# Optimization experiments

Hardware: AMD Instinct MI355X
Metric: run time of the kernel (lower is better)

## Reference

```python
import jax, jax.numpy as jnp
import numpy as np

B, S, H, D, HID = 2, 2048, 16, 64, 512
INTER = 2 * HID
EPS = 1e-8
SCALE = D ** -0.5
ROPE_THETA = 10000.0


def setup_inputs() -> dict:
    key = jax.random.key(0)
    ks = jax.random.split(key, 12)
    x = jax.random.normal(ks[0], (B, S, HID), dtype=jnp.float32)
    # RoPE tables: angles[s, i] = s / theta^(2i/D), half-dim = D//2
    inv_freq = 1.0 / (ROPE_THETA ** (jnp.arange(0, D, 2, dtype=jnp.float32) / D))  # [D/2]
    ang = jnp.arange(S, dtype=jnp.float32)[:, None] * inv_freq[None, :]            # [S, D/2]
    cos_val = jnp.cos(ang)[None, None]  # [1,1,S,D/2]
    sin_val = jnp.sin(ang)[None, None]
    # additive causal mask
    i = jnp.arange(S)
    causal_mask = jnp.where(i[None, :] > i[:, None], -1e9, 0.0).astype(jnp.float32)[None, None]
    std = 0.02
    wq = jax.random.normal(ks[1], (HID, H * D), dtype=jnp.float32) * std
    wk = jax.random.normal(ks[2], (HID, H * D), dtype=jnp.float32) * std
    wv = jax.random.normal(ks[3], (HID, H * D), dtype=jnp.float32) * std
    wo = jax.random.normal(ks[4], (H * D, HID), dtype=jnp.float32) * std
    w_gate = jax.random.normal(ks[5], (HID, INTER), dtype=jnp.float32) * std
    w_up = jax.random.normal(ks[6], (HID, INTER), dtype=jnp.float32) * std
    w_down = jax.random.normal(ks[7], (INTER, HID), dtype=jnp.float32) * std
    norm1_w = jnp.ones((HID,), dtype=jnp.float32)
    norm2_w = jnp.ones((HID,), dtype=jnp.float32)
    ls_attn = jnp.full((HID,), 0.01, dtype=jnp.float32)
    ls_mlp = jnp.full((HID,), 0.01, dtype=jnp.float32)
    return {"x": x, "cos_val": cos_val, "sin_val": sin_val, "causal_mask": causal_mask,
            "wq": wq, "wk": wk, "wv": wv, "wo": wo,
            "w_gate": w_gate, "w_up": w_up, "w_down": w_down,
            "norm1_w": norm1_w, "norm2_w": norm2_w, "ls_attn": ls_attn, "ls_mlp": ls_mlp}


def _rmsnorm(x, w):
    return x * jax.lax.rsqrt(jnp.mean(x * x, axis=-1, keepdims=True) + EPS) * w


def _rope(t, cos_val, sin_val):
    # t: [B,H,S,D]; rotate-half style with concat halves
    t1, t2 = t[..., : D // 2], t[..., D // 2 :]
    return jnp.concatenate([t1 * cos_val - t2 * sin_val, t2 * cos_val + t1 * sin_val], axis=-1)


def reference(x, cos_val, sin_val, causal_mask, wq, wk, wv, wo,
              w_gate, w_up, w_down, norm1_w, norm2_w, ls_attn, ls_mlp):
    residual = x
    h = _rmsnorm(x, norm1_w)  # [B,S,HID]
    q = (h @ wq).reshape(B, S, H, D).transpose(0, 2, 1, 3)  # [B,H,S,D]
    k = (h @ wk).reshape(B, S, H, D).transpose(0, 2, 1, 3)
    v = (h @ wv).reshape(B, S, H, D).transpose(0, 2, 1, 3)
    q = _rope(q, cos_val, sin_val)
    k = _rope(k, cos_val, sin_val)
    scores = jnp.einsum("bhqd,bhkd->bhqk", q, k) * SCALE + causal_mask
    attn = jax.nn.softmax(scores, axis=-1)
    out = jnp.einsum("bhqk,bhkd->bhqd", attn, v)  # [B,H,S,D]
    out = out.transpose(0, 2, 1, 3).reshape(B, S, H * D)
    attn_out = (out @ wo) * ls_attn  # LayerScale == per-channel scale
    h = residual + attn_out
    residual2 = h
    g = _rmsnorm(h, norm2_w)
    m = jax.nn.silu(g @ w_gate) * (g @ w_up)  # SwiGLU
    m = (m @ w_down) * ls_mlp
    return residual2 + m
```

## Files before the change

kernel.cpp:

```cpp
#include <hip/hip_runtime.h>
#include <hip/hip_bf16.h>

typedef __bf16 bf16x8 __attribute__((ext_vector_type(8)));
typedef __bf16 bf16x4 __attribute__((ext_vector_type(4)));
typedef float f32x4 __attribute__((ext_vector_type(4)));

#define SEQ   2048
#define NB    2
#define NTOK  4096
#define HIDD  512
#define NHEAD 16
#define DHEAD 64
#define QKVN  3072
#define GUN   2048

#define OFF_WQKVT  0u
#define OFF_WOT    3145728u
#define OFF_WGUT   4194304u
#define OFF_WDT    6291456u
#define OFF_HB     7340032u
#define OFF_QKV    11534336u
#define OFF_ATTN   36700160u
#define OFF_H2     45088768u
#define OFF_G      53477376u
#define OFF_M      (OFF_QKV + 16777216u)

#define QSCALE 0.1803368801111731f

#if __has_builtin(__builtin_amdgcn_exp2f)
#define EXP2(x) __builtin_amdgcn_exp2f(x)
#else
#define EXP2(x) exp2f(x)
#endif

typedef unsigned int __attribute__((address_space(1))) as1_uint;
typedef unsigned int __attribute__((address_space(3))) as3_uint;
__device__ __forceinline__ void gload16(const void* g, void* l) {
    __builtin_amdgcn_global_load_lds((const as1_uint*)g, (as3_uint*)l, 16, 0, 0);
}

__global__ __launch_bounds__(256) void prep_k(
    const float* __restrict__ wq, const float* __restrict__ wk,
    const float* __restrict__ wv, const float* __restrict__ wo,
    const float* __restrict__ wg, const float* __restrict__ wu,
    const float* __restrict__ wd,
    __bf16* __restrict__ qkvT, __bf16* __restrict__ woT,
    __bf16* __restrict__ wguT, __bf16* __restrict__ wdT,
    const float* __restrict__ x, const float* __restrict__ norm1,
    __bf16* __restrict__ hb) {
    __shared__ float t[32][33];
    int bid = blockIdx.x;
    if (bid < 3584) {
        int which = bid >> 9, bx = bid & 511;
        const float* in; __bf16* out; int K, N, mode = 0, phase = 0;
        switch (which) {
            case 0: in = wq; out = qkvT;              K = 512;  N = 1024; break;
            case 1: in = wk; out = qkvT + 1024 * 512; K = 512;  N = 1024; break;
            case 2: in = wv; out = qkvT + 2048 * 512; K = 512;  N = 1024; break;
            case 3: in = wo; out = woT;               K = 1024; N = 512;  break;
            case 4: in = wg; out = wguT;              K = 512;  N = 1024; mode = 1; phase = 0; break;
            case 5: in = wu; out = wguT;              K = 512;  N = 1024; mode = 1; phase = 1; break;
            default: in = wd; out = wdT;              K = 1024; N = 512;  break;
        }
        int ntn = N >> 5;
        int n0 = (bx & (ntn - 1)) * 32;
        int k0 = (bx / ntn) * 32;
        int tx = threadIdx.x & 31, ty = threadIdx.x >> 5;
#pragma unroll
        for (int j = 0; j < 4; ++j)
            t[ty * 4 + j][tx] = in[(size_t)(k0 + ty * 4 + j) * N + n0 + tx];
        __syncthreads();
#pragma unroll
        for (int j = 0; j < 4; ++j) {
            int n = n0 + ty * 4 + j;
            int row = mode ? (((n >> 4) << 5) + phase * 16 + (n & 15)) : n;
            out[(size_t)row * K + k0 + tx] = (__bf16)t[tx][ty * 4 + j];
        }
    } else {
        int row = bid - 3584;
        int tt = threadIdx.x;
        const float* xr = x + (size_t)row * HIDD;
        float2 v = *(const float2*)&xr[tt * 2];
        float ss = v.x * v.x + v.y * v.y;
#pragma unroll
        for (int off = 32; off >= 1; off >>= 1) ss += __shfl_xor(ss, off);
        if ((tt & 63) == 0) t[0][tt >> 6] = ss;
        __syncthreads();
        float tot = t[0][0] + t[0][1] + t[0][2] + t[0][3];
        float r = rsqrtf(tot * (1.0f / HIDD) + 1e-8f);
        hb[(size_t)row * HIDD + tt * 2]     = (__bf16)(v.x * r * norm1[tt * 2]);
        hb[(size_t)row * HIDD + tt * 2 + 1] = (__bf16)(v.y * r * norm1[tt * 2 + 1]);
    }
}

__global__ __launch_bounds__(256) void rmsnorm_k(const float* __restrict__ x,
                                                 const float* __restrict__ w,
                                                 __bf16* __restrict__ out) {
    int row = blockIdx.x;
    int t = threadIdx.x;
    const float* xr = x + (size_t)row * HIDD;
    float2 v = *(const float2*)&xr[t * 2];
    float ss = v.x * v.x + v.y * v.y;
#pragma unroll
    for (int off = 32; off >= 1; off >>= 1) ss += __shfl_xor(ss, off);
    __shared__ float red[4];
    if ((t & 63) == 0) red[t >> 6] = ss;
    __syncthreads();
    float tot = red[0] + red[1] + red[2] + red[3];
    float r = rsqrtf(tot * (1.0f / HIDD) + 1e-8f);
    out[(size_t)row * HIDD + t * 2]     = (__bf16)(v.x * r * w[t * 2]);
    out[(size_t)row * HIDD + t * 2 + 1] = (__bf16)(v.y * r * w[t * 2 + 1]);
}

template <int EPI, int TM, int TN, int BK>
__global__ __launch_bounds__(256) void gemm_bt(const __bf16* __restrict__ A,
                                               const __bf16* __restrict__ Bt,
                                               int M, int N, int K,
                                               __bf16* __restrict__ Cb,
                                               float* __restrict__ Cf,
                                               const float* __restrict__ resid,
                                               const float* __restrict__ scale,
                                               const float* __restrict__ cosv,
                                               const float* __restrict__ sinv) {
    __shared__ alignas(16) __bf16 As[TM][BK];
    __shared__ alignas(16) __bf16 Bs[TN][BK];
    constexpr int MI = TM / 32, NI = TN / 32;
    constexpr int CPB = BK / 8;
    int m0 = blockIdx.y * TM, n0 = blockIdx.x * TN;
    int tid = threadIdx.x;
    int lane = tid & 63, w = tid >> 6;
    int wm = (w >> 1) * (TM / 2), wn = (w & 1) * (TN / 2);
    int lr = lane & 15, lkg = lane >> 4;
    f32x4 acc[MI][NI] = {};
    int nkt = K / BK;
    for (int kt = 0; kt < nkt; ++kt) {
        __syncthreads();
#pragma unroll
        for (int i = 0; i < (TM * BK) / 2048; ++i) {
            int c = i * 256 + tid;
            int row = c / CPB, ch = c % CPB;
            gload16(&A[(size_t)(m0 + row) * K + kt * BK + ((ch ^ (row & 7)) << 3)],
                    (__bf16*)As + c * 8);
        }
#pragma unroll
        for (int i = 0; i < (TN * BK) / 2048; ++i) {
            int c = i * 256 + tid;
            int row = c / CPB, ch = c % CPB;
            gload16(&Bt[(size_t)(n0 + row) * K + kt * BK + ((ch ^ (row & 7)) << 3)],
                    (__bf16*)Bs + c * 8);
        }
        __syncthreads();
#pragma unroll
        for (int kk = 0; kk < BK / 32; ++kk) {
            bf16x8 af[MI], bfv[NI];
#pragma unroll
            for (int mi = 0; mi < MI; ++mi) {
                int row = wm + mi * 16 + lr;
                af[mi] = *(const bf16x8*)&As[row][(((kk * 4 + lkg) ^ (row & 7)) << 3)];
            }
#pragma unroll
            for (int ni = 0; ni < NI; ++ni) {
                int row = wn + ni * 16 + lr;
                bfv[ni] = *(const bf16x8*)&Bs[row][(((kk * 4 + lkg) ^ (row & 7)) << 3)];
            }
#pragma unroll
            for (int mi = 0; mi < MI; ++mi)
#pragma unroll
                for (int ni = 0; ni < NI; ++ni)
                    acc[mi][ni] = __builtin_amdgcn_mfma_f32_16x16x32_bf16(
                        af[mi], bfv[ni], acc[mi][ni], 0, 0, 0);
        }
    }
    if (EPI == 1) {
        bool do_rope = (n0 + wn) < 2048;
        float qf = (n0 + wn) < 1024 ? QSCALE : 1.0f;
#pragma unroll
        for (int mi = 0; mi < MI; ++mi)
#pragma unroll
            for (int r = 0; r < 4; ++r) {
                int row = m0 + wm + mi * 16 + (lane >> 4) * 4 + r;
                int s = row & (SEQ - 1);
#pragma unroll
                for (int ni = 0; ni < 2; ++ni) {
                    float v1 = acc[mi][ni][r], v2 = acc[mi][ni + 2][r];
                    size_t i1 = (size_t)row * N + n0 + wn + ni * 16 + lr;
                    size_t i2 = i1 + 32;
                    if (do_rope) {
                        int d = ni * 16 + lr;
                        float c = cosv[s * 32 + d], sn = sinv[s * 32 + d];
                        Cb[i1] = (__bf16)((v1 * c - v2 * sn) * qf);
                        Cb[i2] = (__bf16)((v2 * c + v1 * sn) * qf);
                    } else {
                        Cb[i1] = (__bf16)v1;
                        Cb[i2] = (__bf16)v2;
                    }
                }
            }
    } else if (EPI == 3) {
#pragma unroll
        for (int mi = 0; mi < MI; ++mi)
#pragma unroll
            for (int r = 0; r < 4; ++r) {
                int row = m0 + wm + mi * 16 + (lane >> 4) * 4 + r;
#pragma unroll
                for (int ni = 0; ni < 4; ni += 2) {
                    float g = acc[mi][ni][r], u = acc[mi][ni + 1][r];
                    float mv = (g / (1.0f + __expf(-g))) * u;
                    int j = (((n0 + wn + ni * 16) >> 5) << 4) + lr;
                    Cb[(size_t)row * 1024 + j] = (__bf16)mv;
                }
            }
    } else {
#pragma unroll
        for (int mi = 0; mi < MI; ++mi)
#pragma unroll
            for (int ni = 0; ni < NI; ++ni)
#pragma unroll
                for (int r = 0; r < 4; ++r) {
                    int row = m0 + wm + mi * 16 + (lane >> 4) * 4 + r;
                    int col = n0 + wn + ni * 16 + lr;
                    size_t idx = (size_t)row * N + col;
                    float vv = acc[mi][ni][r];
                    if (EPI == 0) Cb[idx] = (__bf16)vv;
                    else          Cf[idx] = resid[idx] + vv * scale[col];
                }
    }
}

__global__ __launch_bounds__(256, 2) void attn_k(const __bf16* __restrict__ qkv,
                                                 __bf16* __restrict__ outp) {
    __shared__ alignas(16) __bf16 KtF[2][128 * 64];
    __shared__ alignas(16) __bf16 VtF[2][64 * 128];
    int bh = blockIdx.x;
    int b = bh >> 4, h = bh & 15;
    int qbA = blockIdx.y;
    int qbB = 31 - qbA;
    int tid = threadIdx.x, lane = tid & 63, w = tid >> 6;
    int lq = lane & 15, g = lane >> 4;
    int qr0A = qbA * 64 + w * 16, qr0B = qbB * 64 + w * 16;
    size_t tokb = (size_t)b * SEQ;
    int lastA = qbA >> 1;
    int nkbB = (qbB >> 1) + 1;

    int vslotA = ((lane >> 5) << 2) + ((lane >> 2) & 3);
    int vkeA   = (((lane >> 4) & 1) << 2) + (lane & 3);
    int vslotB = vslotA + 8;

    bf16x8 ones8;
#pragma unroll
    for (int e = 0; e < 8; ++e) ones8[e] = (__bf16)1.0f;

    bf16x8 aqA[2], aqB[2];
#pragma unroll
    for (int ks = 0; ks < 2; ++ks) {
        aqA[ks] = *(const bf16x8*)&qkv[(tokb + qr0A + lq) * QKVN + h * 64 + ks * 32 + g * 8];
        aqB[ks] = *(const bf16x8*)&qkv[(tokb + qr0B + lq) * QKVN + h * 64 + ks * 32 + g * 8];
    }

    f32x4 oaA[4] = {}, oaB[4] = {};
    f32x4 olA = {}, olB = {};
    uint4 va0, va1, vb0, vb1;
    int cur = 0;

#define STAGE(kbn, buf)                                                                            \
    {                                                                                              \
        _Pragma("unroll")                                                                          \
        for (int i = 0; i < 4; ++i) {                                                              \
            int c = i * 256 + tid;                                                                 \
            int kr = c >> 3, sw = c & 7;                                                           \
            gload16(&qkv[(tokb + (kbn) * 128 + kr) * QKVN + 1024 + h * 64 + ((sw ^ (kr & 7)) << 3)], \
                    &KtF[buf][c * 8]);                                                             \
        }                                                                                          \
        const __bf16* v0p = &qkv[(tokb + (kbn) * 128 + lane) * QKVN + 2048 + h * 64];              \
        const __bf16* v1p = v0p + (size_t)64 * QKVN;                                               \
        va0 = *(const uint4*)(v0p + (w * 2) * 8);                                                  \
        va1 = *(const uint4*)(v0p + (w * 2 + 1) * 8);                                              \
        vb0 = *(const uint4*)(v1p + (w * 2) * 8);                                                  \
        vb1 = *(const uint4*)(v1p + (w * 2 + 1) * 8);                                              \
    }

#define WRITE_V(buf)                                                                  \
    {                                                                                 \
        const __bf16* ea0 = (const __bf16*)&va0;                                      \
        const __bf16* ea1 = (const __bf16*)&va1;                                      \
        const __bf16* eb0 = (const __bf16*)&vb0;                                      \
        const __bf16* eb1 = (const __bf16*)&vb1;                                      \
        _Pragma("unroll")                                                             \
        for (int j = 0; j < 8; ++j) {                                                 \
            int dv0 = (w * 2) * 8 + j, dv1 = (w * 2 + 1) * 8 + j;                     \
            VtF[buf][dv0 * 128 + ((vslotA ^ j) << 3) + vkeA] = ea0[j];                \
            VtF[buf][dv1 * 128 + ((vslotA ^ j) << 3) + vkeA] = ea1[j];                \
            VtF[buf][dv0 * 128 + ((vslotB ^ j) << 3) + vkeA] = eb0[j];                \
            VtF[buf][dv1 * 128 + ((vslotB ^ j) << 3) + vkeA] = eb1[j];                \
        }                                                                             \
    }

#define QK_ONE(sc, aq)                                                                             \
    _Pragma("unroll")                                                                              \
    for (int jt = 0; jt < 8; ++jt)                                                                 \
        _Pragma("unroll")                                                                          \
        for (int ks = 0; ks < 2; ++ks) {                                                           \
            bf16x8 bk = *(const bf16x8*)&KtF[cur][(jt * 16 + lq) * 64 + (((ks * 4 + g) ^ (lq & 7)) << 3)]; \
            sc[jt] = __builtin_amdgcn_mfma_f32_16x16x32_bf16(bk, aq[ks], sc[jt], 0, 0, 0);         \
        }

#define MASK_ONE(sc, qr0_t, kb_t)                                                                  \
    {                                                                                              \
        int qabs = (qr0_t) + lq;                                                                   \
        _Pragma("unroll")                                                                          \
        for (int jt = 0; jt < 8; ++jt)                                                             \
            _Pragma("unroll")                                                                      \
            for (int r = 0; r < 4; ++r) {                                                          \
                int key = (kb_t) * 128 + jt * 16 + g * 4 + r;                                      \
                if (key > qabs) sc[jt][r] = -1e9f;                                                 \
            }                                                                                      \
    }

#define EXP_ONE(sc)                                                                                \
    _Pragma("unroll")                                                                              \
    for (int jt = 0; jt < 8; ++jt)                                                                 \
        _Pragma("unroll")                                                                          \
        for (int r = 0; r < 4; ++r) sc[jt][r] = EXP2(sc[jt][r]);

#define PV_ONE(sc, oa, ol)                                                                         \
    _Pragma("unroll")                                                                              \
    for (int ks2 = 0; ks2 < 4; ++ks2) {                                                            \
        bf16x8 pfv;                                                                                \
        _Pragma("unroll")                                                                          \
        for (int e = 0; e < 4; ++e) {                                                              \
            pfv[e]     = (__bf16)sc[2 * ks2][e];                                                   \
            pfv[e + 4] = (__bf16)sc[2 * ks2 + 1][e];                                               \
        }                                                                                          \
        ol = __builtin_amdgcn_mfma_f32_16x16x32_bf16(ones8, pfv, ol, 0, 0, 0);                     \
        _Pragma("unroll")                                                                          \
        for (int dt = 0; dt < 4; ++dt) {                                                           \
            bf16x8 av = *(const bf16x8*)&VtF[cur][(dt * 16 + lq) * 128 + (((ks2 * 4 + g) ^ (lq & 7)) << 3)]; \
            oa[dt] = __builtin_amdgcn_mfma_f32_16x16x32_bf16(av, pfv, oa[dt], 0, 0, 0);            \
        }                                                                                          \
    }

    STAGE(0, 0);
    WRITE_V(0);
    __syncthreads();

    for (int kb = 0; kb <= lastA; ++kb) {
        STAGE(kb + 1, cur ^ 1);
        {
            f32x4 scA[8] = {}, scB[8] = {};
            __builtin_amdgcn_s_setprio(1);
#pragma unroll
            for (int jt = 0; jt < 8; ++jt)
#pragma unroll
                for (int ks = 0; ks < 2; ++ks) {
                    bf16x8 bk = *(const bf16x8*)&KtF[cur][(jt * 16 + lq) * 64 + (((ks * 4 + g) ^ (lq & 7)) << 3)];
                    scB[jt] = __builtin_amdgcn_mfma_f32_16x16x32_bf16(bk, aqB[ks], scB[jt], 0, 0, 0);
                    scA[jt] = __builtin_amdgcn_mfma_f32_16x16x32_bf16(bk, aqA[ks], scA[jt], 0, 0, 0);
                }
            __builtin_amdgcn_s_setprio(0);
            if (kb == lastA) MASK_ONE(scA, qr0A, kb);
            EXP_ONE(scB);
            EXP_ONE(scA);
            __builtin_amdgcn_s_setprio(1);
#pragma unroll
            for (int ks2 = 0; ks2 < 4; ++ks2) {
                bf16x8 pfvA, pfvB;
#pragma unroll
                for (int e = 0; e < 4; ++e) {
                    pfvB[e]     = (__bf16)scB[2 * ks2][e];
                    pfvB[e + 4] = (__bf16)scB[2 * ks2 + 1][e];
                    pfvA[e]     = (__bf16)scA[2 * ks2][e];
                    pfvA[e + 4] = (__bf16)scA[2 * ks2 + 1][e];
                }
                olB = __builtin_amdgcn_mfma_f32_16x16x32_bf16(ones8, pfvB, olB, 0, 0, 0);
                olA = __builtin_amdgcn_mfma_f32_16x16x32_bf16(ones8, pfvA, olA, 0, 0, 0);
#pragma unroll
                for (int dt = 0; dt < 4; ++dt) {
                    bf16x8 av = *(const bf16x8*)&VtF[cur][(dt * 16 + lq) * 128 + (((ks2 * 4 + g) ^ (lq & 7)) << 3)];
                    oaB[dt] = __builtin_amdgcn_mfma_f32_16x16x32_bf16(av, pfvB, oaB[dt], 0, 0, 0);
                    oaA[dt] = __builtin_amdgcn_mfma_f32_16x16x32_bf16(av, pfvA, oaA[dt], 0, 0, 0);
                }
            }
            __builtin_amdgcn_s_setprio(0);
        }
        WRITE_V(cur ^ 1);
        __syncthreads();
        cur ^= 1;
    }
    for (int kb = lastA + 1; kb < nkbB; ++kb) {
        bool pf = (kb + 1) < nkbB;
        if (pf) STAGE(kb + 1, cur ^ 1);
        {
            f32x4 sc[8] = {};
            __builtin_amdgcn_s_setprio(1);
            QK_ONE(sc, aqB);
            __builtin_amdgcn_s_setprio(0);
            if (kb == (qbB >> 1)) MASK_ONE(sc, qr0B, kb);
            EXP_ONE(sc);
            __builtin_amdgcn_s_setprio(1);
            PV_ONE(sc, oaB, olB);
            __builtin_amdgcn_s_setprio(0);
        }
        if (pf) WRITE_V(cur ^ 1);
        __syncthreads();
        cur ^= 1;
    }

    float invA = 1.0f / olA[0], invB = 1.0f / olB[0];
#pragma unroll
    for (int dt = 0; dt < 4; ++dt) {
        bf16x4 ovA, ovB;
#pragma unroll
        for (int r = 0; r < 4; ++r) {
            ovA[r] = (__bf16)(oaA[dt][r] * invA);
            ovB[r] = (__bf16)(oaB[dt][r] * invB);
        }
        *(bf16x4*)&outp[(tokb + qr0A + lq) * 1024 + h * 64 + dt * 16 + g * 4] = ovA;
        *(bf16x4*)&outp[(tokb + qr0B + lq) * 1024 + h * 64 + dt * 16 + g * 4] = ovB;
    }
#undef STAGE
#undef WRITE_V
#undef QK_ONE
#undef MASK_ONE
#undef EXP_ONE
#undef PV_ONE
}

extern "C" void kernel_launch(void* const* d_in, const int* in_sizes, int n_in,
                              void* d_out, int out_size, void* d_ws, size_t ws_size,
                              hipStream_t stream) {
    const float* x       = (const float*)d_in[0];
    const float* cosv    = (const float*)d_in[1];
    const float* sinv    = (const float*)d_in[2];
    const float* wq      = (const float*)d_in[4];
    const float* wk      = (const float*)d_in[5];
    const float* wv      = (const float*)d_in[6];
    const float* wo      = (const float*)d_in[7];
    const float* wgate   = (const float*)d_in[8];
    const float* wup     = (const float*)d_in[9];
    const float* wdown   = (const float*)d_in[10];
    const float* norm1   = (const float*)d_in[11];
    const float* norm2   = (const float*)d_in[12];
    const float* ls_attn = (const float*)d_in[13];
    const float* ls_mlp  = (const float*)d_in[14];

    char* ws = (char*)d_ws;
    __bf16* wqkvT = (__bf16*)(ws + OFF_WQKVT);
    __bf16* woT   = (__bf16*)(ws + OFF_WOT);
    __bf16* wguT  = (__bf16*)(ws + OFF_WGUT);
    __bf16* wdT   = (__bf16*)(ws + OFF_WDT);
    __bf16* hb    = (__bf16*)(ws + OFF_HB);
    __bf16* qkvb  = (__bf16*)(ws + OFF_QKV);
    __bf16* attnb = (__bf16*)(ws + OFF_ATTN);
    float*  h2    = (float*)(ws + OFF_H2);
    __bf16* gb    = (__bf16*)(ws + OFF_G);
    __bf16* mb    = (__bf16*)(ws + OFF_M);
    float*  outf  = (float*)d_out;

    prep_k<<<7680, 256, 0, stream>>>(
        wq, wk, wv, wo, wgate, wup, wdown, wqkvT, woT, wguT, wdT, x, norm1, hb);
    gemm_bt<1, 128, 128, 64><<<dim3(QKVN / 128, NTOK / 128), 256, 0, stream>>>(
        hb, wqkvT, NTOK, QKVN, 512, qkvb, nullptr, nullptr, nullptr, cosv, sinv);
    attn_k<<<dim3(NB * NHEAD, 16), 256, 0, stream>>>(qkvb, attnb);
    gemm_bt<2, 64, 64, 128><<<dim3(HIDD / 64, NTOK / 64), 256, 0, stream>>>(
        attnb, woT, NTOK, HIDD, 1024, nullptr, h2, x, ls_attn, nullptr, nullptr);
    rmsnorm_k<<<NTOK, 256, 0, stream>>>(h2, norm2, gb);
    gemm_bt<3, 128, 128, 64><<<dim3(GUN / 128, NTOK / 128), 256, 0, stream>>>(
        gb, wguT, NTOK, GUN, 512, mb, nullptr, nullptr, nullptr, nullptr, nullptr);
    gemm_bt<2, 64, 64, 128><<<dim3(HIDD / 64, NTOK / 64), 256, 0, stream>>>(
        mb, wdT, NTOK, HIDD, 1024, nullptr, outf, h2, ls_mlp, nullptr, nullptr);
}
```

Before: 122.6 us.

## Load K fragments directly into registers instead of staging through LDS

The attention kernel drops the shared-memory K tile. Each wave now loads its K MFMA operands straight from global memory into registers (kf[8][2]), prefetched one block ahead, while V still goes through double-buffered LDS. The two query-tile loops are merged into a single loop that processes tile B and then, conditionally, tile A, using a raw s_barrier with an lgkmcnt wait. This removes the LDS write and read traffic for K and halves LDS use, but every wave redundantly loads the full K block from global or L2 and register pressure rises, which may lower occupancy.

```diff
diff --git a/kernel.cpp b/kernel.cpp
--- a/kernel.cpp
+++ b/kernel.cpp
@@ -229,7 +229,6 @@
 
 __global__ __launch_bounds__(256, 2) void attn_k(const __bf16* __restrict__ qkv,
                                                  __bf16* __restrict__ outp) {
-    __shared__ alignas(16) __bf16 KtF[2][128 * 64];
     __shared__ alignas(16) __bf16 VtF[2][64 * 128];
     int bh = blockIdx.x;
     int b = bh >> 4, h = bh & 15;
@@ -257,20 +256,22 @@
         aqB[ks] = *(const bf16x8*)&qkv[(tokb + qr0B + lq) * QKVN + h * 64 + ks * 32 + g * 8];
     }
 
+    bf16x8 kf[8][2];
     f32x4 oaA[4] = {}, oaB[4] = {};
     f32x4 olA = {}, olB = {};
     uint4 va0, va1, vb0, vb1;
     int cur = 0;
 
-#define STAGE(kbn, buf)                                                                            \
+#define LOAD_K(kbn)                                                                                \
+    _Pragma("unroll")                                                                              \
+    for (int jt = 0; jt < 8; ++jt)                                                                 \
+        _Pragma("unroll")                                                                          \
+        for (int ks = 0; ks < 2; ++ks)                                                             \
+            kf[jt][ks] = *(const bf16x8*)&qkv[(tokb + (kbn) * 128 + jt * 16 + lq) * QKVN + 1024    \
+                                              + h * 64 + ks * 32 + g * 8];
+
+#define LOAD_V(kbn)                                                                                \
     {                                                                                              \
-        _Pragma("unroll")                                                                          \
-        for (int i = 0; i < 4; ++i) {                                                              \
-            int c = i * 256 + tid;                                                                 \
-            int kr = c >> 3, sw = c & 7;                                                           \
-            gload16(&qkv[(tokb + (kbn) * 128 + kr) * QKVN + 1024 + h * 64 + ((sw ^ (kr & 7)) << 3)], \
-                    &KtF[buf][c * 8]);                                                             \
-        }                                                                                          \
         const __bf16* v0p = &qkv[(tokb + (kbn) * 128 + lane) * QKVN + 2048 + h * 64];              \
         const __bf16* v1p = v0p + (size_t)64 * QKVN;                                               \
         va0 = *(const uint4*)(v0p + (w * 2) * 8);                                                  \
@@ -295,14 +296,16 @@
         }                                                                             \
     }
 
-#define QK_ONE(sc, aq)                                                                             \
-    _Pragma("unroll")                                                                              \
-    for (int jt = 0; jt < 8; ++jt)                                                                 \
+#define QK_R(sc, aq)                                                                               \
+    {                                                                                              \
+        __builtin_amdgcn_s_setprio(1);                                                             \
         _Pragma("unroll")                                                                          \
-        for (int ks = 0; ks < 2; ++ks) {                                                           \
-            bf16x8 bk = *(const bf16x8*)&KtF[cur][(jt * 16 + lq) * 64 + (((ks * 4 + g) ^ (lq & 7)) << 3)]; \
-            sc[jt] = __builtin_amdgcn_mfma_f32_16x16x32_bf16(bk, aq[ks], sc[jt], 0, 0, 0);         \
-        }
+        for (int jt = 0; jt < 8; ++jt)                                                             \
+            _Pragma("unroll")                                                                      \
+            for (int ks = 0; ks < 2; ++ks)                                                         \
+                sc[jt] = __builtin_amdgcn_mfma_f32_16x16x32_bf16(kf[jt][ks], aq[ks], sc[jt], 0, 0, 0); \
+        __builtin_amdgcn_s_setprio(0);                                                             \
+    }
 
 #define MASK_ONE(sc, qr0_t, kb_t)                                                                  \
     {                                                                                              \
@@ -323,85 +326,57 @@
         for (int r = 0; r < 4; ++r) sc[jt][r] = EXP2(sc[jt][r]);
 
 #define PV_ONE(sc, oa, ol)                                                                         \
-    _Pragma("unroll")                                                                              \
-    for (int ks2 = 0; ks2 < 4; ++ks2) {                                                            \
-        bf16x8 pfv;                                                                                \
+    {                                                                                              \
+        __builtin_amdgcn_s_setprio(1);                                                             \
         _Pragma("unroll")                                                                          \
-        for (int e = 0; e < 4; ++e) {                                                              \
-            pfv[e]     = (__bf16)sc[2 * ks2][e];                                                   \
-            pfv[e + 4] = (__bf16)sc[2 * ks2 + 1][e];                                               \
+        for (int ks2 = 0; ks2 < 4; ++ks2) {                                                        \
+            bf16x8 pfv;                                                                            \
+            _Pragma("unroll")                                                                      \
+            for (int e = 0; e < 4; ++e) {                                                          \
+                pfv[e]     = (__bf16)sc[2 * ks2][e];                                               \
+                pfv[e + 4] = (__bf16)sc[2 * ks2 + 1][e];                                           \
+            }                                                                                      \
+            ol = __builtin_amdgcn_mfma_f32_16x16x32_bf16(ones8, pfv, ol, 0, 0, 0);                 \
+            _Pragma("unroll")                                                                      \
+            for (int dt = 0; dt < 4; ++dt) {                                                       \
+                bf16x8 av = *(const bf16x8*)&VtF[cur][(dt * 16 + lq) * 128 + (((ks2 * 4 + g) ^ (lq & 7)) << 3)]; \
+                oa[dt] = __builtin_amdgcn_mfma_f32_16x16x32_bf16(av, pfv, oa[dt], 0, 0, 0);        \
+            }                                                                                      \
         }                                                                                          \
-        ol = __builtin_amdgcn_mfma_f32_16x16x32_bf16(ones8, pfv, ol, 0, 0, 0);                     \
-        _Pragma("unroll")                                                                          \
-        for (int dt = 0; dt < 4; ++dt) {                                                           \
-            bf16x8 av = *(const bf16x8*)&VtF[cur][(dt * 16 + lq) * 128 + (((ks2 * 4 + g) ^ (lq & 7)) << 3)]; \
-            oa[dt] = __builtin_amdgcn_mfma_f32_16x16x32_bf16(av, pfv, oa[dt], 0, 0, 0);            \
-        }                                                                                          \
-    }
-
-    STAGE(0, 0);
+        __builtin_amdgcn_s_setprio(0);                                                             \
+    }
+
+    LOAD_K(0);
+    LOAD_V(0);
     WRITE_V(0);
-    __syncthreads();
-
-    for (int kb = 0; kb <= lastA; ++kb) {
-        STAGE(kb + 1, cur ^ 1);
-        {
-            f32x4 scA[8] = {}, scB[8] = {};
-            __builtin_amdgcn_s_setprio(1);
-#pragma unroll
-            for (int jt = 0; jt < 8; ++jt)
-#pragma unroll
-                for (int ks = 0; ks < 2; ++ks) {
-                    bf16x8 bk = *(const bf16x8*)&KtF[cur][(jt * 16 + lq) * 64 + (((ks * 4 + g) ^ (lq & 7)) << 3)];
-                    scB[jt] = __builtin_amdgcn_mfma_f32_16x16x32_bf16(bk, aqB[ks], scB[jt], 0, 0, 0);
-                    scA[jt] = __builtin_amdgcn_mfma_f32_16x16x32_bf16(bk, aqA[ks], scA[jt], 0, 0, 0);
-                }
-            __builtin_amdgcn_s_setprio(0);
-            if (kb == lastA) MASK_ONE(scA, qr0A, kb);
-            EXP_ONE(scB);
-            EXP_ONE(scA);
-            __builtin_amdgcn_s_setprio(1);
-#pragma unroll
-            for (int ks2 = 0; ks2 < 4; ++ks2) {
-                bf16x8 pfvA, pfvB;
-#pragma unroll
-                for (int e = 0; e < 4; ++e) {
-                    pfvB[e]     = (__bf16)scB[2 * ks2][e];
-                    pfvB[e + 4] = (__bf16)scB[2 * ks2 + 1][e];
-                    pfvA[e]     = (__bf16)scA[2 * ks2][e];
-                    pfvA[e + 4] = (__bf16)scA[2 * ks2 + 1][e];
-                }
-                olB = __builtin_amdgcn_mfma_f32_16x16x32_bf16(ones8, pfvB, olB, 0, 0, 0);
-                olA = __builtin_amdgcn_mfma_f32_16x16x32_bf16(ones8, pfvA, olA, 0, 0, 0);
-#pragma unroll
-                for (int dt = 0; dt < 4; ++dt) {
-                    bf16x8 av = *(const bf16x8*)&VtF[cur][(dt * 16 + lq) * 128 + (((ks2 * 4 + g) ^ (lq & 7)) << 3)];
-                    oaB[dt] = __builtin_amdgcn_mfma_f32_16x16x32_bf16(av, pfvB, oaB[dt], 0, 0, 0);
-                    oaA[dt] = __builtin_amdgcn_mfma_f32_16x16x32_bf16(av, pfvA, oaA[dt], 0, 0, 0);
-                }
-            }
-            __builtin_amdgcn_s_setprio(0);
-        }
-        WRITE_V(cur ^ 1);
-        __syncthreads();
-        cur ^= 1;
-    }
-    for (int kb = lastA + 1; kb < nkbB; ++kb) {
+    asm volatile("s_waitcnt lgkmcnt(0)" ::: "memory");
+    __builtin_amdgcn_s_barrier();
+    __builtin_amdgcn_sched_barrier(0);
+
+    for (int kb = 0; kb < nkbB; ++kb) {
         bool pf = (kb + 1) < nkbB;
-        if (pf) STAGE(kb + 1, cur ^ 1);
+        if (pf) LOAD_V(kb + 1);
         {
             f32x4 sc[8] = {};
-            __builtin_amdgcn_s_setprio(1);
-            QK_ONE(sc, aqB);
-            __builtin_amdgcn_s_setprio(0);
-            if (kb == (qbB >> 1)) MASK_ONE(sc, qr0B, kb);
+            QK_R(sc, aqB);
+            if (kb == nkbB - 1) MASK_ONE(sc, qr0B, kb);
             EXP_ONE(sc);
-            __builtin_amdgcn_s_setprio(1);
             PV_ONE(sc, oaB, olB);
-            __builtin_amdgcn_s_setprio(0);
-        }
-        if (pf) WRITE_V(cur ^ 1);
-        __syncthreads();
+        }
+        if (kb <= lastA) {
+            f32x4 sc[8] = {};
+            QK_R(sc, aqA);
+            if (kb == lastA) MASK_ONE(sc, qr0A, kb);
+            EXP_ONE(sc);
+            PV_ONE(sc, oaA, olA);
+        }
+        if (pf) {
+            LOAD_K(kb + 1);
+            WRITE_V(cur ^ 1);
+        }
+        asm volatile("s_waitcnt lgkmcnt(0)" ::: "memory");
+        __builtin_amdgcn_s_barrier();
+        __builtin_amdgcn_sched_barrier(0);
         cur ^= 1;
     }
 
@@ -417,9 +392,10 @@
         *(bf16x4*)&outp[(tokb + qr0A + lq) * 1024 + h * 64 + dt * 16 + g * 4] = ovA;
         *(bf16x4*)&outp[(tokb + qr0B + lq) * 1024 + h * 64 + dt * 16 + g * 4] = ovB;
     }
-#undef STAGE
+#undef LOAD_K
+#undef LOAD_V
 #undef WRITE_V
-#undef QK_ONE
+#undef QK_R
 #undef MASK_ONE
 #undef EXP_ONE
 #undef PV_ONE
```

Result: slower. 156.4 us (+27.5%).
